# Kernel tuning notes

Hardware: AMD Instinct MI355X
Metric: run time of the kernel (lower is better)

The kernel has to match this reference:

```python
import jax, jax.numpy as jnp
import numpy as np

EPS = 1e-5

def _layer_norm(x, gamma, beta):
    mu = jnp.mean(x, axis=-1, keepdims=True)
    var = jnp.mean(jnp.square(x - mu), axis=-1, keepdims=True)
    return (x - mu) * jax.lax.rsqrt(var + EPS) * gamma + beta

def setup_inputs() -> dict:
    key = jax.random.key(0)
    ks = jax.random.split(key, 4)
    B, S, D, F = 4, 2048, 1024, 4096
    return {
        "hidden_state": jax.random.normal(ks[0], (B, S, D), dtype=jnp.float32),
        "attention_mask": jnp.zeros((B, S), dtype=jnp.float32),
        "w1": jax.random.normal(ks[1], (D, F), dtype=jnp.float32) * (1.0 / np.sqrt(D)),
        "b1": jnp.zeros((F,), dtype=jnp.float32),
        "w2": jax.random.normal(ks[2], (F, D), dtype=jnp.float32) * (1.0 / np.sqrt(F)),
        "b2": jnp.zeros((D,), dtype=jnp.float32),
        "ln1_gamma": jnp.ones((D,), dtype=jnp.float32),
        "ln1_beta": jnp.zeros((D,), dtype=jnp.float32),
        "ln2_gamma": jnp.ones((D,), dtype=jnp.float32),
        "ln2_beta": jnp.zeros((D,), dtype=jnp.float32),
    }

def reference(hidden_state, attention_mask, w1, b1, w2, b2,
              ln1_gamma, ln1_beta, ln2_gamma, ln2_beta):
    h = hidden_state
    d = h.shape[-1]
    # Self-attention with Q=K=V=h (no projections), single head.
    scores = jnp.einsum("bqd,bkd->bqk", h, h) / jnp.sqrt(jnp.float32(d))
    scores = scores + attention_mask[:, None, :]  # additive mask [B,1,S]
    probs = jax.nn.softmax(scores, axis=-1)
    attn_out = jnp.einsum("bqk,bkd->bqd", probs, h)
    # Residual + post-LN (dropout inactive in eval)
    h = _layer_norm(h + attn_out, ln1_gamma, ln1_beta)
    # FFN: Linear -> exact GELU -> Linear
    ffn = jax.nn.gelu(h @ w1 + b1, approximate=False) @ w2 + b2
    h = _layer_norm(h + ffn, ln2_gamma, ln2_beta)
    return h
```

## Files before the change

### kernel.cpp

```cpp
#include <hip/hip_runtime.h>
#include <hip/hip_bf16.h>
#include <math.h>

typedef __bf16 bf16;
typedef __bf16 bf16x8 __attribute__((ext_vector_type(8)));
typedef float  f32x4  __attribute__((ext_vector_type(4)));

__device__ __forceinline__ float gelu_f(float x) {
    return 0.5f * x * (1.0f + erff(x * 0.70710678118654752440f));
}

__global__ void detect_k(const unsigned short* __restrict__ h, int* __restrict__ flag)
{
    if (threadIdx.x == 0 && blockIdx.x == 0) {
        int cnt = 0;
        for (int i = 0; i < 256; i += 2) {
            int e = (h[i] >> 7) & 0xFF;
            cnt += (e >= 100 && e <= 140) ? 1 : 0;
        }
        *flag = (cnt >= 96) ? 0 : 1;
    }
}

struct SmallConvArgs {
    const void* src[7];
    bf16* dst[7];
    int n[7];
};
__global__ __launch_bounds__(256) void small_convert_k(SmallConvArgs a,
                                                       const int* __restrict__ flag)
{
    const int seg = blockIdx.y;
    const int i = blockIdx.x * 256 + threadIdx.x;
    if (i >= a.n[seg]) return;
    const float v = (*flag) ? ((const float*)a.src[seg])[i]
                            : (float)((const bf16*)a.src[seg])[i];
    a.dst[seg][i] = (bf16)v;
}

__global__ __launch_bounds__(256) void conv_transpose_k(
    const void* __restrict__ in, bf16* __restrict__ outT,
    int R, int C, const int* __restrict__ flag)
{
    __shared__ bf16 tile[32][33];
    const int c0 = blockIdx.x * 32;
    const int r0 = blockIdx.y * 32;
    const int tx = threadIdx.x & 31;
    const int ty = threadIdx.x >> 5;
    const bool f32 = (*flag) != 0;
#pragma unroll
    for (int i = 0; i < 32; i += 8) {
        const long idx = (long)(r0 + ty + i) * C + (c0 + tx);
        const float v = f32 ? ((const float*)in)[idx] : (float)((const bf16*)in)[idx];
        tile[ty + i][tx] = (bf16)v;
    }
    __syncthreads();
#pragma unroll
    for (int i = 0; i < 32; i += 8)
        outT[(long)(c0 + ty + i) * R + (r0 + tx)] = tile[tx][ty + i];
}

__global__ __launch_bounds__(256) void conv_transpose_h_k(
    const void* __restrict__ in, bf16* __restrict__ h_bf, bf16* __restrict__ hT,
    int S, int D, const int* __restrict__ flag)
{
    __shared__ bf16 tile[32][33];
    const long sB = (long)S * D;
    const int d0 = blockIdx.x * 32;
    const int s0 = blockIdx.y * 32;
    const int b  = blockIdx.z;
    const int tx = threadIdx.x & 31;
    const int ty = threadIdx.x >> 5;
    const bool f32 = (*flag) != 0;
#pragma unroll
    for (int i = 0; i < 32; i += 8) {
        const long idx = b * sB + (long)(s0 + ty + i) * D + (d0 + tx);
        const float v = f32 ? ((const float*)in)[idx] : (float)((const bf16*)in)[idx];
        const bf16 bv = (bf16)v;
        h_bf[idx] = bv;
        tile[ty + i][tx] = bv;
    }
    __syncthreads();
#pragma unroll
    for (int i = 0; i < 32; i += 8)
        hT[b * sB + (long)(d0 + ty + i) * S + (s0 + tx)] = tile[tx][ty + i];
}

__device__ __forceinline__ void gll16(const bf16* g, bf16* l)
{
    __builtin_amdgcn_global_load_lds(
        (const __attribute__((address_space(1))) void*)g,
        (__attribute__((address_space(3))) void*)l, 16, 0, 0);
}

template <int MODE, int BM, int BN>
__global__ __launch_bounds__(512, 2) void gemm_big(
    const bf16* __restrict__ A, const bf16* __restrict__ Bt,
    bf16* __restrict__ C, const bf16* __restrict__ bias,
    int M, int N, int K, float scale,
    long sA, long sB, long sC)
{
    constexpr int WM = BM / 2;
    constexpr int WN = BN / 4;
    constexpr int MI = WM / 16;
    constexpr int NI = WN / 16;

    A  += (long)blockIdx.z * sA;
    Bt += (long)blockIdx.z * sB;
    C  += (long)blockIdx.z * sC;

    const int tileM = blockIdx.y * BM;
    const int tileN = blockIdx.x * BN;

    __shared__ __align__(16) bf16 As0[BM * 64];
    __shared__ __align__(16) bf16 As1[BM * 64];
    __shared__ __align__(16) bf16 Bs0[BN * 64];
    __shared__ __align__(16) bf16 Bs1[BN * 64];

    const int t    = threadIdx.x;
    const int lane = t & 63;
    const int wave = t >> 6;
    const int wr   = wave >> 2;
    const int wc   = wave & 3;
    const int quad = lane >> 4;
    const int l16  = lane & 15;

    const int srow   = lane >> 3;
    const int lchunk = ((lane & 7) - srow) & 7;

    f32x4 acc[MI][NI] = {};

    auto swz = [](int row, int chunk) { return row * 64 + (((chunk + row) & 7) * 8); };

    auto stage = [&](bf16* as, bf16* bs, int k0) {
#pragma unroll
        for (int r2 = 0; r2 < BM / 64; ++r2) {
            const int unit = wave * (BM / 64) + r2;
            const int row  = unit * 8 + srow;
            gll16(A + (long)(tileM + row) * K + (k0 + lchunk * 8), as + unit * 512);
        }
#pragma unroll
        for (int r2 = 0; r2 < BN / 64; ++r2) {
            const int unit = wave * (BN / 64) + r2;
            const int row  = unit * 8 + srow;
            gll16(Bt + (long)(tileN + row) * K + (k0 + lchunk * 8), bs + unit * 512);
        }
    };

    auto compute = [&](const bf16* as, const bf16* bs) {
#pragma unroll
        for (int kk = 0; kk < 64; kk += 32) {
            const int chunk = (kk >> 3) + quad;
            bf16x8 af[MI], bfr[NI];
#pragma unroll
            for (int i = 0; i < MI; ++i)
                af[i] = *(const bf16x8*)&as[swz(wr * WM + i * 16 + l16, chunk)];
#pragma unroll
            for (int j = 0; j < NI; ++j)
                bfr[j] = *(const bf16x8*)&bs[swz(wc * WN + j * 16 + l16, chunk)];
#pragma unroll
            for (int mi = 0; mi < MI; ++mi)
#pragma unroll
                for (int ni = 0; ni < NI; ++ni)
                    acc[mi][ni] = __builtin_amdgcn_mfma_f32_16x16x32_bf16(
                        af[mi], bfr[ni], acc[mi][ni], 0, 0, 0);
        }
    };

    stage(As0, Bs0, 0);
    __syncthreads();
    for (int u = 0; u < K / 64; u += 2) {
        const int k1 = (u + 1) * 64;
        const int k2 = (u + 2) * 64;
        if (k1 < K) stage(As1, Bs1, k1);
        compute(As0, Bs0);
        __syncthreads();
        if (k1 < K) {
            if (k2 < K) stage(As0, Bs0, k2);
            compute(As1, Bs1);
            __syncthreads();
        }
    }

#pragma unroll
    for (int mi = 0; mi < MI; ++mi) {
        const int rbase = tileM + wr * WM + mi * 16 + quad * 4;
#pragma unroll
        for (int ni = 0; ni < NI; ++ni) {
            const int col = tileN + wc * WN + ni * 16 + l16;
            float bv = 0.0f;
            if (MODE >= 2) bv = (float)bias[col];
#pragma unroll
            for (int r = 0; r < 4; ++r) {
                float v = acc[mi][ni][r];
                if (MODE == 0) v *= scale;
                if (MODE >= 2) v += bv;
                if (MODE == 2) v = gelu_f(v);
                C[(long)(rbase + r) * N + col] = (bf16)v;
            }
        }
    }
}

__global__ __launch_bounds__(256) void softmax_k(
    bf16* __restrict__ scores, const bf16* __restrict__ mask, int S)
{
    const long rowOff = ((long)blockIdx.y * S + blockIdx.x) * S;
    bf16* row = scores + rowOff;
    const bf16* mrow = mask + (long)blockIdx.y * S;
    const int t = threadIdx.x;

    const bf16x8 r = ((const bf16x8*)row)[t];
    const bf16x8 m = ((const bf16x8*)mrow)[t];
    float v[8];
    float mx = -1e30f;
#pragma unroll
    for (int i = 0; i < 8; ++i) {
        v[i] = (float)r[i] + (float)m[i];
        mx = fmaxf(mx, v[i]);
    }
#pragma unroll
    for (int off = 32; off > 0; off >>= 1)
        mx = fmaxf(mx, __shfl_down(mx, off));
    __shared__ float redm[4];
    if ((t & 63) == 0) redm[t >> 6] = mx;
    __syncthreads();
    mx = fmaxf(fmaxf(redm[0], redm[1]), fmaxf(redm[2], redm[3]));

    float s = 0.0f;
#pragma unroll
    for (int i = 0; i < 8; ++i) { v[i] = __expf(v[i] - mx); s += v[i]; }
#pragma unroll
    for (int off = 32; off > 0; off >>= 1)
        s += __shfl_down(s, off);
    __shared__ float reds[4];
    if ((t & 63) == 0) reds[t >> 6] = s;
    __syncthreads();
    s = reds[0] + reds[1] + reds[2] + reds[3];
    const float inv = 1.0f / s;
    bf16x8 o;
#pragma unroll
    for (int i = 0; i < 8; ++i) o[i] = (bf16)(v[i] * inv);
    ((bf16x8*)row)[t] = o;
}

__global__ __launch_bounds__(128) void ln_residual_k(
    const bf16* __restrict__ x1, const bf16* __restrict__ x2,
    const bf16* __restrict__ gamma, const bf16* __restrict__ beta,
    bf16* __restrict__ out)
{
    constexpr int D = 1024;
    const long off = (long)blockIdx.x * D;
    const int t = threadIdx.x;
    const bf16x8 a = ((const bf16x8*)(x1 + off))[t];
    const bf16x8 b = ((const bf16x8*)(x2 + off))[t];
    float v[8];
    float s = 0.0f, s2 = 0.0f;
#pragma unroll
    for (int i = 0; i < 8; ++i) {
        v[i] = (float)a[i] + (float)b[i];
        s  += v[i];
        s2 += v[i] * v[i];
    }
#pragma unroll
    for (int o2 = 32; o2 > 0; o2 >>= 1) {
        s  += __shfl_down(s, o2);
        s2 += __shfl_down(s2, o2);
    }
    __shared__ float rs[2], rs2[2];
    if ((t & 63) == 0) { rs[t >> 6] = s; rs2[t >> 6] = s2; }
    __syncthreads();
    s  = rs[0] + rs[1];
    s2 = rs2[0] + rs2[1];
    const float mean = s / (float)D;
    const float var  = s2 / (float)D - mean * mean;
    const float inv  = rsqrtf(var + 1e-5f);
    const bf16x8 g  = ((const bf16x8*)gamma)[t];
    const bf16x8 be = ((const bf16x8*)beta)[t];
    bf16x8 o;
#pragma unroll
    for (int i = 0; i < 8; ++i)
        o[i] = (bf16)((v[i] - mean) * inv * (float)g[i] + (float)be[i]);
    ((bf16x8*)(out + off))[t] = o;
}

__global__ __launch_bounds__(128) void ln_out_k(
    const bf16* __restrict__ x1, const bf16* __restrict__ x2,
    const bf16* __restrict__ gamma, const bf16* __restrict__ beta,
    void* __restrict__ outv, const int* __restrict__ flag)
{
    constexpr int D = 1024;
    const long off = (long)blockIdx.x * D;
    const int t = threadIdx.x;
    const bf16x8 a = ((const bf16x8*)(x1 + off))[t];
    const bf16x8 b = ((const bf16x8*)(x2 + off))[t];
    float v[8];
    float s = 0.0f, s2 = 0.0f;
#pragma unroll
    for (int i = 0; i < 8; ++i) {
        v[i] = (float)a[i] + (float)b[i];
        s  += v[i];
        s2 += v[i] * v[i];
    }
#pragma unroll
    for (int o2 = 32; o2 > 0; o2 >>= 1) {
        s  += __shfl_down(s, o2);
        s2 += __shfl_down(s2, o2);
    }
    __shared__ float rs[2], rs2[2];
    if ((t & 63) == 0) { rs[t >> 6] = s; rs2[t >> 6] = s2; }
    __syncthreads();
    s  = rs[0] + rs[1];
    s2 = rs2[0] + rs2[1];
    const float mean = s / (float)D;
    const float var  = s2 / (float)D - mean * mean;
    const float inv  = rsqrtf(var + 1e-5f);
    const bf16x8 g  = ((const bf16x8*)gamma)[t];
    const bf16x8 be = ((const bf16x8*)beta)[t];
    if (*flag) {
        f32x4 o1, o2v;
#pragma unroll
        for (int i = 0; i < 4; ++i) {
            o1[i]  = (v[i] - mean) * inv * (float)g[i] + (float)be[i];
            o2v[i] = (v[4 + i] - mean) * inv * (float)g[4 + i] + (float)be[4 + i];
        }
        f32x4* op = (f32x4*)((float*)outv + off);
        op[t * 2]     = o1;
        op[t * 2 + 1] = o2v;
    } else {
        bf16x8 o;
#pragma unroll
        for (int i = 0; i < 8; ++i)
            o[i] = (bf16)((v[i] - mean) * inv * (float)g[i] + (float)be[i]);
        ((bf16x8*)((bf16*)outv + off))[t] = o;
    }
}

extern "C" void kernel_launch(void* const* d_in, const int* in_sizes, int n_in,
                              void* d_out, int out_size, void* d_ws, size_t ws_size,
                              hipStream_t stream)
{
    constexpr int B = 4, S = 2048, D = 1024, F = 4096;
    constexpr long MB = 1024 * 1024;

    const void* h_raw  = d_in[0];
    const void* mk_raw = d_in[1];
    const void* w1_raw = d_in[2];
    const void* b1_raw = d_in[3];
    const void* w2_raw = d_in[4];
    const void* b2_raw = d_in[5];
    const void* g1_raw = d_in[6];
    const void* be1_raw= d_in[7];
    const void* g2_raw = d_in[8];
    const void* be2_raw= d_in[9];

    char* ws = (char*)d_ws;
    bf16* scores = (bf16*)(ws + 0);
    bf16* gact   = (bf16*)(ws + 0);
    bf16* hT     = (bf16*)(ws + 32 * MB);
    bf16* h_bf   = (bf16*)(ws + 48 * MB);
    bf16* y1     = (bf16*)(ws + 64 * MB);
    bf16* w1T    = (bf16*)(ws + 80 * MB);
    bf16* w2T    = (bf16*)(ws + 88 * MB);
    bf16* axf    = (bf16*)(ws + 96 * MB);
    char* sm     = ws + 112 * MB;
    int*  flag   = (int*)(sm);
    bf16* mk_bf  = (bf16*)(sm + 1024);
    bf16* b1_bf  = (bf16*)(sm + 17408 + 1024);
    bf16* b2_bf  = (bf16*)(sm + 25600 + 3072);
    bf16* g1_bf  = (bf16*)(sm + 27648 + 3072);
    bf16* be1_bf = (bf16*)(sm + 29696 + 3072);
    bf16* g2_bf  = (bf16*)(sm + 31744 + 3072);
    bf16* be2_bf = (bf16*)(sm + 33792 + 3072);

    const long SD = (long)S * D;
    const long SS = (long)S * S;

    detect_k<<<1, 64, 0, stream>>>((const unsigned short*)h_raw, flag);

    SmallConvArgs sca;
    sca.src[0] = mk_raw;  sca.dst[0] = mk_bf;  sca.n[0] = B * S;
    sca.src[1] = b1_raw;  sca.dst[1] = b1_bf;  sca.n[1] = F;
    sca.src[2] = b2_raw;  sca.dst[2] = b2_bf;  sca.n[2] = D;
    sca.src[3] = g1_raw;  sca.dst[3] = g1_bf;  sca.n[3] = D;
    sca.src[4] = be1_raw; sca.dst[4] = be1_bf; sca.n[4] = D;
    sca.src[5] = g2_raw;  sca.dst[5] = g2_bf;  sca.n[5] = D;
    sca.src[6] = be2_raw; sca.dst[6] = be2_bf; sca.n[6] = D;
    small_convert_k<<<dim3((B * S) / 256, 7), 256, 0, stream>>>(sca, flag);

    conv_transpose_h_k<<<dim3(D / 32, S / 32, B), 256, 0, stream>>>(
        h_raw, h_bf, hT, S, D, flag);

    conv_transpose_k<<<dim3(F / 32, D / 32), 256, 0, stream>>>(w1_raw, w1T, D, F, flag);
    conv_transpose_k<<<dim3(D / 32, F / 32), 256, 0, stream>>>(w2_raw, w2T, F, D, flag);

    gemm_big<0, 256, 256><<<dim3(S / 256, S / 256, B), 512, 0, stream>>>(
        h_bf, h_bf, scores, nullptr, S, S, D, 0.03125f, SD, SD, SS);

    softmax_k<<<dim3(S, B), 256, 0, stream>>>(scores, mk_bf, S);

    gemm_big<1, 256, 128><<<dim3(D / 128, S / 256, B), 512, 0, stream>>>(
        scores, hT, axf, nullptr, S, D, S, 1.0f, SS, SD, SD);

    ln_residual_k<<<B * S, 128, 0, stream>>>(h_bf, axf, g1_bf, be1_bf, y1);

    gemm_big<2, 256, 256><<<dim3(F / 256, (B * S) / 256, 1), 512, 0, stream>>>(
        y1, w1T, gact, b1_bf, B * S, F, D, 1.0f, 0, 0, 0);

    gemm_big<3, 256, 128><<<dim3(D / 128, (B * S) / 256, 1), 512, 0, stream>>>(
        gact, w2T, axf, b2_bf, B * S, D, F, 1.0f, 0, 0, 0);

    ln_out_k<<<B * S, 128, 0, stream>>>(y1, axf, g2_bf, be2_bf, d_out, flag);
}
```

Measured before the change: 443.1 us.

## Add software-pipelined GEMM with manual LDS reads and vmcnt-controlled prefetch

Adds a new 256x256 GEMM kernel that hand-schedules each K step. It issues inline ds_read_b128 LDS reads, then waits with explicit lgkmcnt and vmcnt, and uses raw s_barrier calls so the global-to-LDS prefetch two steps ahead overlaps the MFMA work. It replaces the generic kernel for the QK^T scores GEMM and the FFN first-layer GEMM. The aim is to hide global load latency and cut synchronization stalls, at the cost of fragile hand-written waitcnt and barrier ordering.

```diff
diff --git a/kernel.cpp b/kernel.cpp
--- a/kernel.cpp
+++ b/kernel.cpp
@@ -5,6 +5,7 @@
 typedef __bf16 bf16;
 typedef __bf16 bf16x8 __attribute__((ext_vector_type(8)));
 typedef float  f32x4  __attribute__((ext_vector_type(4)));
+typedef int    i32x4  __attribute__((ext_vector_type(4)));
 
 __device__ __forceinline__ float gelu_f(float x) {
     return 0.5f * x * (1.0f + erff(x * 0.70710678118654752440f));
@@ -92,6 +93,15 @@
         (const __attribute__((address_space(1))) void*)g,
         (__attribute__((address_space(3))) void*)l, 16, 0, 0);
 }
+
+__device__ __forceinline__ bf16x8 lds_read_b128(unsigned addr)
+{
+    i32x4 r;
+    asm volatile("ds_read_b128 %0, %1" : "=v"(r) : "v"(addr));
+    return __builtin_bit_cast(bf16x8, r);
+}
+
+#define LDS_ADDR(p) ((unsigned)(unsigned long long)(const __attribute__((address_space(3))) void*)(p))
 
 template <int MODE, int BM, int BN>
 __global__ __launch_bounds__(512, 2) void gemm_big(
@@ -180,6 +190,141 @@
             compute(As1, Bs1);
             __syncthreads();
         }
+    }
+
+#pragma unroll
+    for (int mi = 0; mi < MI; ++mi) {
+        const int rbase = tileM + wr * WM + mi * 16 + quad * 4;
+#pragma unroll
+        for (int ni = 0; ni < NI; ++ni) {
+            const int col = tileN + wc * WN + ni * 16 + l16;
+            float bv = 0.0f;
+            if (MODE >= 2) bv = (float)bias[col];
+#pragma unroll
+            for (int r = 0; r < 4; ++r) {
+                float v = acc[mi][ni][r];
+                if (MODE == 0) v *= scale;
+                if (MODE >= 2) v += bv;
+                if (MODE == 2) v = gelu_f(v);
+                C[(long)(rbase + r) * N + col] = (bf16)v;
+            }
+        }
+    }
+}
+
+template <int MODE>
+__global__ __launch_bounds__(512, 2) void gemm_pipe(
+    const bf16* __restrict__ A, const bf16* __restrict__ Bt,
+    bf16* __restrict__ C, const bf16* __restrict__ bias,
+    int M, int N, int K, float scale,
+    long sA, long sB, long sC)
+{
+    constexpr int BM = 256, BN = 256;
+    constexpr int WM = BM / 2;
+    constexpr int WN = BN / 4;
+    constexpr int MI = WM / 16;
+    constexpr int NI = WN / 16;
+
+    A  += (long)blockIdx.z * sA;
+    Bt += (long)blockIdx.z * sB;
+    C  += (long)blockIdx.z * sC;
+
+    const int tileM = blockIdx.y * BM;
+    const int tileN = blockIdx.x * BN;
+
+    __shared__ __align__(16) bf16 As0[BM * 64];
+    __shared__ __align__(16) bf16 As1[BM * 64];
+    __shared__ __align__(16) bf16 Bs0[BN * 64];
+    __shared__ __align__(16) bf16 Bs1[BN * 64];
+
+    const int t    = threadIdx.x;
+    const int lane = t & 63;
+    const int wave = t >> 6;
+    const int wr   = wave >> 2;
+    const int wc   = wave & 3;
+    const int quad = lane >> 4;
+    const int l16  = lane & 15;
+
+    const int srow   = lane >> 3;
+    const int lchunk = ((lane & 7) - srow) & 7;
+
+    const int NK = K >> 6;
+
+    f32x4 acc[MI][NI] = {};
+
+    auto swz = [](int row, int chunk) { return row * 64 + (((chunk + row) & 7) * 8); };
+
+    auto stage = [&](bf16* as, bf16* bs, int k0) {
+#pragma unroll
+        for (int r2 = 0; r2 < 4; ++r2) {
+            const int unit = wave * 4 + r2;
+            const int row  = unit * 8 + srow;
+            gll16(A + (long)(tileM + row) * K + (k0 + lchunk * 8), as + unit * 512);
+        }
+#pragma unroll
+        for (int r2 = 0; r2 < 4; ++r2) {
+            const int unit = wave * 4 + r2;
+            const int row  = unit * 8 + srow;
+            gll16(Bt + (long)(tileN + row) * K + (k0 + lchunk * 8), bs + unit * 512);
+        }
+    };
+
+    auto iter = [&](bf16* as, bf16* bs, int u) {
+        const unsigned ab = LDS_ADDR(as);
+        const unsigned bb = LDS_ADDR(bs);
+        {
+            bf16x8 af[MI], bfv[NI];
+#pragma unroll
+            for (int i = 0; i < MI; ++i)
+                af[i] = lds_read_b128(ab + 2u * (unsigned)swz(wr * WM + i * 16 + l16, quad));
+#pragma unroll
+            for (int j = 0; j < NI; ++j)
+                bfv[j] = lds_read_b128(bb + 2u * (unsigned)swz(wc * WN + j * 16 + l16, quad));
+            asm volatile("s_waitcnt lgkmcnt(0)" ::: "memory");
+            __builtin_amdgcn_sched_barrier(0);
+#pragma unroll
+            for (int mi = 0; mi < MI; ++mi)
+#pragma unroll
+                for (int ni = 0; ni < NI; ++ni)
+                    acc[mi][ni] = __builtin_amdgcn_mfma_f32_16x16x32_bf16(
+                        af[mi], bfv[ni], acc[mi][ni], 0, 0, 0);
+        }
+        {
+            bf16x8 af[MI], bfv[NI];
+#pragma unroll
+            for (int i = 0; i < MI; ++i)
+                af[i] = lds_read_b128(ab + 2u * (unsigned)swz(wr * WM + i * 16 + l16, 4 + quad));
+#pragma unroll
+            for (int j = 0; j < NI; ++j)
+                bfv[j] = lds_read_b128(bb + 2u * (unsigned)swz(wc * WN + j * 16 + l16, 4 + quad));
+            asm volatile("s_waitcnt lgkmcnt(0)" ::: "memory");
+            __builtin_amdgcn_sched_barrier(0);
+            __builtin_amdgcn_s_barrier();
+            const int k2 = (u + 2) << 6;
+            if (k2 < K) stage(as, bs, k2);
+            __builtin_amdgcn_sched_barrier(0);
+#pragma unroll
+            for (int mi = 0; mi < MI; ++mi)
+#pragma unroll
+                for (int ni = 0; ni < NI; ++ni)
+                    acc[mi][ni] = __builtin_amdgcn_mfma_f32_16x16x32_bf16(
+                        af[mi], bfv[ni], acc[mi][ni], 0, 0, 0);
+            if (u + 1 < NK) {
+                if (k2 < K) asm volatile("s_waitcnt vmcnt(8)" ::: "memory");
+                else        asm volatile("s_waitcnt vmcnt(0)" ::: "memory");
+                __builtin_amdgcn_s_barrier();
+            }
+        }
+    };
+
+    stage(As0, Bs0, 0);
+    stage(As1, Bs1, 64);
+    asm volatile("s_waitcnt vmcnt(8)" ::: "memory");
+    __builtin_amdgcn_s_barrier();
+
+    for (int u = 0; u < NK; u += 2) {
+        iter(As0, Bs0, u);
+        iter(As1, Bs1, u + 1);
     }
 
 #pragma unroll
@@ -394,7 +539,7 @@
     conv_transpose_k<<<dim3(F / 32, D / 32), 256, 0, stream>>>(w1_raw, w1T, D, F, flag);
     conv_transpose_k<<<dim3(D / 32, F / 32), 256, 0, stream>>>(w2_raw, w2T, F, D, flag);
 
-    gemm_big<0, 256, 256><<<dim3(S / 256, S / 256, B), 512, 0, stream>>>(
+    gemm_pipe<0><<<dim3(S / 256, S / 256, B), 512, 0, stream>>>(
         h_bf, h_bf, scores, nullptr, S, S, D, 0.03125f, SD, SD, SS);
 
     softmax_k<<<dim3(S, B), 256, 0, stream>>>(scores, mk_bf, S);
@@ -404,7 +549,7 @@
 
     ln_residual_k<<<B * S, 128, 0, stream>>>(h_bf, axf, g1_bf, be1_bf, y1);
 
-    gemm_big<2, 256, 256><<<dim3(F / 256, (B * S) / 256, 1), 512, 0, stream>>>(
+    gemm_pipe<2><<<dim3(F / 256, (B * S) / 256, 1), 512, 0, stream>>>(
         y1, w1T, gact, b1_bf, B * S, F, D, 1.0f, 0, 0, 0);
 
     gemm_big<3, 256, 128><<<dim3(D / 128, (B * S) / 256, 1), 512, 0, stream>>>(
```

New measurement: 784.6 us. +77.1%, slower.
